# Kernel tuning notes

Hardware: AMD Instinct MI355X
Metric: run time of the kernel (lower is better)

The kernel has to match this reference:

```python
import jax, jax.numpy as jnp
import numpy as np

D_MODEL = 2048
N_HEADS = 16
N_KV_HEADS = 4
HEAD_DIM = D_MODEL // N_HEADS
KV_DIM = N_KV_HEADS * HEAD_DIM
EPS = 1e-6


def setup_inputs() -> dict:
    key = jax.random.key(0)
    ks = jax.random.split(key, 5)
    N, L = 4, 2048
    x = jax.random.normal(ks[0], (N, L, D_MODEL), dtype=jnp.float32)
    Wqkv = jax.random.normal(ks[1], (D_MODEL, D_MODEL + 2 * KV_DIM), dtype=jnp.float32) * (1.0 / np.sqrt(D_MODEL))
    bqkv = jnp.zeros((D_MODEL + 2 * KV_DIM,), dtype=jnp.float32)
    Wout = jax.random.normal(ks[2], (D_MODEL, D_MODEL), dtype=jnp.float32) * (1.0 / np.sqrt(D_MODEL))
    bout = jnp.zeros((D_MODEL,), dtype=jnp.float32)
    q_scale = jnp.ones((HEAD_DIM,), dtype=jnp.float32)
    k_scale = jnp.ones((HEAD_DIM,), dtype=jnp.float32)
    return {"x": x, "Wqkv": Wqkv, "bqkv": bqkv, "q_scale": q_scale, "k_scale": k_scale, "Wout": Wout, "bout": bout}


def _rmsnorm(x, scale):
    return x * (scale / jnp.sqrt(jnp.mean(jnp.square(x), axis=-1, keepdims=True) + EPS))


def reference(x, Wqkv, bqkv, q_scale, k_scale, Wout, bout):
    N, L, D = x.shape
    qkv = x @ Wqkv + bqkv  # [N, L, D + 2*kv_dim]
    q = qkv[..., :D].reshape(N, L, N_HEADS, HEAD_DIM).transpose(0, 2, 1, 3)          # [N,H,L,hd]
    k = qkv[..., D:D + KV_DIM].reshape(N, L, N_KV_HEADS, HEAD_DIM).transpose(0, 2, 1, 3)  # [N,Hkv,L,hd]
    v = qkv[..., D + KV_DIM:].reshape(N, L, N_KV_HEADS, HEAD_DIM).transpose(0, 2, 1, 3)
    q = _rmsnorm(q, q_scale)
    k = _rmsnorm(k, k_scale)
    # GQA expand (repeat_interleave over head dim)
    n_rep = N_HEADS // N_KV_HEADS
    k = jnp.repeat(k, n_rep, axis=1)
    v = jnp.repeat(v, n_rep, axis=1)
    scale = 1.0 / jnp.sqrt(jnp.float32(HEAD_DIM))
    scores = jnp.einsum("nhqd,nhkd->nhqk", q, k) * scale  # [N,H,L,L]
    causal = jnp.tril(jnp.ones((L, L), dtype=bool))
    scores = jnp.where(causal, scores, jnp.finfo(scores.dtype).min)
    attn = jax.nn.softmax(scores, axis=-1)
    y = jnp.einsum("nhqk,nhkd->nhqd", attn, v)  # [N,H,L,hd]
    y = y.transpose(0, 2, 1, 3).reshape(N, L, D)
    return y @ Wout + bout
```

## Files before the change

kernel.cpp:

```cpp
#include <hip/hip_runtime.h>

typedef unsigned int uint_t;
typedef unsigned short ushort_t;

using f32x4 = __attribute__((ext_vector_type(4))) float;
using bf16x8 = __attribute__((ext_vector_type(8))) short;

#define D_MODEL 2048
#define N_HEADS 16
#define N_KV    4
#define HD      128
#define KV_DIM  (N_KV * HD)
#define NQKV    (D_MODEL + 2*KV_DIM)
#define SEQ     2048
#define NB      4
#define MROWS   (NB * SEQ)
#define SM_SCALE 0.08838834764831845f

__device__ __forceinline__ ushort_t f2bf(float f) {
    uint_t u = __float_as_uint(f);
    u = (u + 0x7FFFu + ((u >> 16) & 1u)) >> 16;
    return (ushort_t)u;
}
__device__ __forceinline__ float bf2f(ushort_t h) {
    return __uint_as_float(((uint_t)h) << 16);
}

__device__ __forceinline__ void gload16(const ushort_t* g, ushort_t* l) {
    __builtin_amdgcn_global_load_lds(
        (const __attribute__((address_space(1))) unsigned int*)g,
        (__attribute__((address_space(3))) unsigned int*)l, 16, 0, 0);
}

__global__ __launch_bounds__(256) void conv_x_kernel(const float* __restrict__ in,
                                                     ushort_t* __restrict__ out, int n) {
    int i = (blockIdx.x * 256 + threadIdx.x) * 4;
    if (i >= n) return;
    float4 v = *(const float4*)&in[i];
    ushort_t o[4] = {f2bf(v.x), f2bf(v.y), f2bf(v.z), f2bf(v.w)};
    *(uint2*)&out[i] = *(uint2*)o;
}

__global__ __launch_bounds__(256) void conv_wt_kernel(const float* __restrict__ W,
                                                      ushort_t* __restrict__ WT,
                                                      int K, int Nout) {
    __shared__ float tile[32][33];
    int n0 = blockIdx.x * 32, k0 = blockIdx.y * 32;
    int tx = threadIdx.x, ty = threadIdx.y;
    for (int i = 0; i < 4; ++i)
        tile[ty + 8*i][tx] = W[(size_t)(k0 + ty + 8*i) * Nout + n0 + tx];
    __syncthreads();
    for (int i = 0; i < 4; ++i)
        WT[(size_t)(n0 + ty + 8*i) * K + k0 + tx] = f2bf(tile[tx][ty + 8*i]);
}

__global__ __launch_bounds__(256) void vt_kernel(const ushort_t* __restrict__ qkv,
                                                 ushort_t* __restrict__ Vt) {
    __shared__ ushort_t tile[64][72];
    int l0 = blockIdx.x * 64, d0 = blockIdx.y * 64;
    int nk = blockIdx.z;
    int n = nk >> 2, kvh = nk & 3;
    int t = threadIdx.x;
    const int coff = 2560 + kvh * 128 + d0;
    for (int i = 0; i < 2; ++i) {
        int idx = t + i * 256;
        int rr = idx >> 3, c = idx & 7;
        uint4 v = *(const uint4*)&qkv[(size_t)(n * SEQ + l0 + rr) * NQKV + coff + c * 8];
        *(uint4*)&tile[rr][c * 8] = v;
    }
    __syncthreads();
    for (int i = 0; i < 2; ++i) {
        int idx = t + i * 256;
        int dr = idx >> 3, c2 = idx & 7;
        ushort_t o[8];
        for (int j = 0; j < 8; ++j) o[j] = tile[c2 * 8 + j][dr];
        *(uint4*)&Vt[((size_t)nk * HD + d0 + dr) * SEQ + l0 + c2 * 8] = *(uint4*)o;
    }
}

template <bool OUT_BF16>
__global__ __launch_bounds__(256) void gemm_bt_kernel(const ushort_t* __restrict__ A,
                                                      const ushort_t* __restrict__ BT,
                                                      const float* __restrict__ bias,
                                                      void* __restrict__ C,
                                                      int M, int N, int K) {
    __shared__ ushort_t As[128][64];
    __shared__ ushort_t Bs[128][64];
    const int bm = blockIdx.x * 128, bn = blockIdx.y * 128;
    const int t = threadIdx.x;
    const int w = t >> 6, lane = t & 63, quad = lane >> 4, r = lane & 15;
    const int mb = (w >> 1) * 64, nb = (w & 1) * 64;

    f32x4 acc[4][4] = {};

    for (int k0 = 0; k0 < K; k0 += 64) {
        for (int i = 0; i < 4; ++i) {
            int ci = (w * 4 + i) * 64 + lane;
            int row = ci >> 3, c = ci & 7, cg = c ^ (row & 7);
            gload16(&A [(size_t)(bm + row) * K + k0 + cg * 8], &As[0][0] + (w * 4 + i) * 512);
            gload16(&BT[(size_t)(bn + row) * K + k0 + cg * 8], &Bs[0][0] + (w * 4 + i) * 512);
        }
        __syncthreads();
        for (int kk = 0; kk < 64; kk += 32) {
            bf16x8 af[4], bfr[4];
            int k4 = kk >> 3;
            for (int i = 0; i < 4; ++i)
                af[i]  = *(const bf16x8*)&As[mb + i * 16 + r][((k4 + quad) ^ (r & 7)) * 8];
            for (int j = 0; j < 4; ++j)
                bfr[j] = *(const bf16x8*)&Bs[nb + j * 16 + r][((k4 + quad) ^ (r & 7)) * 8];
            for (int i = 0; i < 4; ++i)
                for (int j = 0; j < 4; ++j)
                    acc[i][j] = __builtin_amdgcn_mfma_f32_16x16x32_bf16(af[i], bfr[j], acc[i][j], 0, 0, 0);
        }
        __syncthreads();
    }
    for (int i = 0; i < 4; ++i)
        for (int j = 0; j < 4; ++j)
            for (int reg = 0; reg < 4; ++reg) {
                int row = bm + mb + i * 16 + quad * 4 + reg;
                int col = bn + nb + j * 16 + r;
                float v = acc[i][j][reg] + bias[col];
                if (OUT_BF16) ((ushort_t*)C)[(size_t)row * N + col] = f2bf(v);
                else          ((float*)C)[(size_t)row * N + col] = v;
            }
}

__global__ __launch_bounds__(256) void rms_rearrange_kernel(const ushort_t* __restrict__ qkv,
                                                            const float* __restrict__ q_scale,
                                                            const float* __restrict__ k_scale,
                                                            ushort_t* __restrict__ Q,
                                                            ushort_t* __restrict__ Kb) {
    int rid = blockIdx.x;
    int n = rid >> 11, l = rid & 2047;
    int w = threadIdx.x >> 6, lane = threadIdx.x & 63;
    const ushort_t* rowp = qkv + (size_t)rid * NQKV;
    int d0 = lane * 2;
    for (int g = w; g < 20; g += 4) {
        uint_t pair = *(const uint_t*)&rowp[g * 128 + d0];
        float v0 = bf2f((ushort_t)(pair & 0xffff));
        float v1 = bf2f((ushort_t)(pair >> 16));
        float ss = v0 * v0 + v1 * v1;
        for (int m = 1; m < 64; m <<= 1) ss += __shfl_xor(ss, m);
        float inv = rsqrtf(ss * (1.0f / 128.0f) + 1e-6f);
        ushort_t* base;
        size_t dst;
        if (g < 16) {
            inv *= SM_SCALE;
            v0 *= inv * q_scale[d0];
            v1 *= inv * q_scale[d0 + 1];
            base = Q;  dst = (((size_t)(n * 16 + g) * SEQ + l) * HD + d0);
        } else {
            v0 *= inv * k_scale[d0];
            v1 *= inv * k_scale[d0 + 1];
            base = Kb; dst = (((size_t)(n * 4 + (g - 16)) * SEQ + l) * HD + d0);
        }
        uint_t op = (uint_t)f2bf(v0) | ((uint_t)f2bf(v1) << 16);
        *(uint_t*)&base[dst] = op;
    }
}

__global__ __launch_bounds__(256, 4) void attn_kernel(const ushort_t* __restrict__ Q,
                                                      const ushort_t* __restrict__ K,
                                                      const ushort_t* __restrict__ Vt,
                                                      ushort_t* __restrict__ Y) {
    const int pid = blockIdx.x, h = blockIdx.y, n = blockIdx.z;
    const int kvh = h >> 2;
    const ushort_t* Qp = Q  + (size_t)(n * N_HEADS + h) * SEQ * HD;
    const ushort_t* Kp = K  + (size_t)(n * N_KV + kvh) * SEQ * HD;
    const ushort_t* Vp = Vt + (size_t)(n * N_KV + kvh) * HD * SEQ;

    __shared__ ushort_t Ks[64][128];
    __shared__ ushort_t Vts[128][64];
    __shared__ ushort_t Ps[64][64];

    const int t = threadIdx.x, w = t >> 6, lane = t & 63, quad = lane >> 4, r = lane & 15;

    for (int rep = 0; rep < 2; ++rep) {
        const int qt = rep ? (31 - pid) : pid;
        __syncthreads();
        for (int i = 0; i < 4; ++i) {
            int ci = (w * 4 + i) * 64 + lane;
            int row = ci >> 4, c = ci & 15, cg = c ^ (row & 7);
            gload16(&Qp[(size_t)(qt * 64 + row) * HD + cg * 8], &Ks[0][0] + (w * 4 + i) * 512);
        }
        __syncthreads();
        bf16x8 aq[4];
        for (int kc = 0; kc < 4; ++kc)
            aq[kc] = *(const bf16x8*)&Ks[w * 16 + r][((kc * 4 + quad) ^ (r & 7)) * 8];

        f32x4 oacc[8] = {};
        float lsum[4] = {0.f, 0.f, 0.f, 0.f};

        for (int ct = 0; ct <= qt; ++ct) {
            __syncthreads();
            for (int i = 0; i < 4; ++i) {
                int ci = (w * 4 + i) * 64 + lane;
                {
                    int row = ci >> 4, c = ci & 15, cg = c ^ (row & 7);
                    gload16(&Kp[(size_t)(ct * 64 + row) * HD + cg * 8], &Ks[0][0] + (w * 4 + i) * 512);
                }
                {
                    int row = ci >> 3, c = ci & 7, cg = c ^ (row & 7);
                    gload16(&Vp[(size_t)row * SEQ + ct * 64 + cg * 8], &Vts[0][0] + (w * 4 + i) * 512);
                }
            }
            __syncthreads();

            f32x4 sacc[4] = {};
            for (int kc = 0; kc < 4; ++kc)
                for (int jt = 0; jt < 4; ++jt) {
                    bf16x8 bk = *(const bf16x8*)&Ks[jt * 16 + r][((kc * 4 + quad) ^ (r & 7)) * 8];
                    sacc[jt] = __builtin_amdgcn_mfma_f32_16x16x32_bf16(aq[kc], bk, sacc[jt], 0, 0, 0);
                }

            const bool diag = (ct == qt);
            for (int reg = 0; reg < 4; ++reg) {
                int prow = w * 16 + quad * 4 + reg;
                int qrow = prow;
                float rsum = 0.f;
                for (int jt = 0; jt < 4; ++jt) {
                    float s = sacc[jt][reg];
                    if (diag && (jt * 16 + r) > qrow) s = -1e30f;
                    float p = __expf(s);
                    ushort_t pb = f2bf(p);
                    rsum += bf2f(pb);
                    Ps[prow][(jt * 16 + r) ^ (quad << 4)] = pb;
                }
                lsum[reg] += rsum;
            }

            for (int kk = 0; kk < 64; kk += 32) {
                int prow = w * 16 + r;
                bf16x8 pa = *(const bf16x8*)&Ps[prow][(kk + quad * 8) ^ ((((r >> 2) & 3)) << 4)];
                for (int dt = 0; dt < 8; ++dt) {
                    bf16x8 bv = *(const bf16x8*)&Vts[dt * 16 + r][(((kk >> 3) + quad) ^ (r & 7)) * 8];
                    oacc[dt] = __builtin_amdgcn_mfma_f32_16x16x32_bf16(pa, bv, oacc[dt], 0, 0, 0);
                }
            }
        }

        for (int reg = 0; reg < 4; ++reg) {
            float s = lsum[reg];
            for (int m = 1; m < 16; m <<= 1) s += __shfl_xor(s, m);
            float invl = 1.0f / s;
            int lrow = qt * 64 + w * 16 + quad * 4 + reg;
            size_t base = ((size_t)(n * SEQ + lrow)) * D_MODEL + h * HD;
            for (int dt = 0; dt < 8; ++dt)
                Y[base + dt * 16 + r] = f2bf(oacc[dt][reg] * invl);
        }
    }
}

extern "C" void kernel_launch(void* const* d_in, const int* in_sizes, int n_in,
                              void* d_out, int out_size, void* d_ws, size_t ws_size,
                              hipStream_t stream) {
    const float* x       = (const float*)d_in[0];
    const float* Wqkv    = (const float*)d_in[1];
    const float* bqkv    = (const float*)d_in[2];
    const float* q_scale = (const float*)d_in[3];
    const float* k_scale = (const float*)d_in[4];
    const float* Wout    = (const float*)d_in[5];
    const float* bout    = (const float*)d_in[6];
    float* out = (float*)d_out;

    ushort_t* xb  = (ushort_t*)d_ws;
    ushort_t* WT  = xb  + (size_t)MROWS * D_MODEL;
    ushort_t* qkv = WT  + (size_t)NQKV * D_MODEL;
    ushort_t* Qb  = qkv + (size_t)MROWS * NQKV;
    ushort_t* Kb  = Qb  + (size_t)NB * N_HEADS * SEQ * HD;
    ushort_t* Vtb = Kb  + (size_t)NB * N_KV * SEQ * HD;

    conv_x_kernel<<<MROWS * D_MODEL / 1024, 256, 0, stream>>>(x, xb, MROWS * D_MODEL);
    conv_wt_kernel<<<dim3(NQKV / 32, D_MODEL / 32), dim3(32, 8), 0, stream>>>(Wqkv, WT, D_MODEL, NQKV);
    gemm_bt_kernel<true><<<dim3(MROWS / 128, NQKV / 128), 256, 0, stream>>>(xb, WT, bqkv, qkv, MROWS, NQKV, D_MODEL);
    rms_rearrange_kernel<<<MROWS, 256, 0, stream>>>(qkv, q_scale, k_scale, Qb, Kb);
    vt_kernel<<<dim3(SEQ / 64, HD / 64, NB * N_KV), 256, 0, stream>>>(qkv, Vtb);
    conv_wt_kernel<<<dim3(D_MODEL / 32, D_MODEL / 32), dim3(32, 8), 0, stream>>>(Wout, WT, D_MODEL, D_MODEL);
    attn_kernel<<<dim3(16, N_HEADS, NB), 256, 0, stream>>>(Qb, Kb, Vtb, xb);
    gemm_bt_kernel<false><<<dim3(MROWS / 128, D_MODEL / 128), 256, 0, stream>>>(xb, WT, bout, out, MROWS, D_MODEL, D_MODEL);
}
```

Measured before the change: 500.7 us.

## Fuse RMSNorm into QKV GEMM epilogue and widen attention Q tile to 128 rows

The QKV GEMM epilogue now adds the bias, computes per-head RMS norms across the two column-warps through shared memory, and writes Q, K and an untransposed V straight into head-major buffers. This removes the separate rms_rearrange pass and the round trip of the full bf16 qkv buffer. The attention kernel now handles 128 query rows per block, with each warp owning two 16-row slices, so every K/V tile loaded into LDS is reused twice. In exchange it uses more registers and lowers the occupancy hint to 2, and the row sum now uses the unrounded fp32 p values instead of the bf16-rounded ones.

Measured after the change: 474.9 us. 1.05x faster.

```diff
diff --git a/kernel.cpp b/kernel.cpp
--- a/kernel.cpp
+++ b/kernel.cpp
@@ -21,9 +21,6 @@
     uint_t u = __float_as_uint(f);
     u = (u + 0x7FFFu + ((u >> 16) & 1u)) >> 16;
     return (ushort_t)u;
-}
-__device__ __forceinline__ float bf2f(ushort_t h) {
-    return __uint_as_float(((uint_t)h) << 16);
 }
 
 __device__ __forceinline__ void gload16(const ushort_t* g, ushort_t* l) {
@@ -54,18 +51,16 @@
         WT[(size_t)(n0 + ty + 8*i) * K + k0 + tx] = f2bf(tile[tx][ty + 8*i]);
 }
 
-__global__ __launch_bounds__(256) void vt_kernel(const ushort_t* __restrict__ qkv,
+__global__ __launch_bounds__(256) void vt_kernel(const ushort_t* __restrict__ Vn,
                                                  ushort_t* __restrict__ Vt) {
     __shared__ ushort_t tile[64][72];
     int l0 = blockIdx.x * 64, d0 = blockIdx.y * 64;
     int nk = blockIdx.z;
-    int n = nk >> 2, kvh = nk & 3;
     int t = threadIdx.x;
-    const int coff = 2560 + kvh * 128 + d0;
     for (int i = 0; i < 2; ++i) {
         int idx = t + i * 256;
         int rr = idx >> 3, c = idx & 7;
-        uint4 v = *(const uint4*)&qkv[(size_t)(n * SEQ + l0 + rr) * NQKV + coff + c * 8];
+        uint4 v = *(const uint4*)&Vn[((size_t)nk * SEQ + l0 + rr) * HD + d0 + c * 8];
         *(uint4*)&tile[rr][c * 8] = v;
     }
     __syncthreads();
@@ -78,11 +73,33 @@
     }
 }
 
-template <bool OUT_BF16>
+#define GEMM_MAIN_LOOP(A, BT, K)                                                   \
+    for (int k0 = 0; k0 < K; k0 += 64) {                                           \
+        for (int i = 0; i < 4; ++i) {                                              \
+            int ci = (w * 4 + i) * 64 + lane;                                      \
+            int row = ci >> 3, c = ci & 7, cg = c ^ (row & 7);                     \
+            gload16(&A [(size_t)(bm + row) * K + k0 + cg * 8], &As[0][0] + (w * 4 + i) * 512); \
+            gload16(&BT[(size_t)(bn + row) * K + k0 + cg * 8], &Bs[0][0] + (w * 4 + i) * 512); \
+        }                                                                          \
+        __syncthreads();                                                           \
+        for (int kk = 0; kk < 64; kk += 32) {                                      \
+            bf16x8 af[4], bfr[4];                                                  \
+            int k4 = kk >> 3;                                                      \
+            for (int i = 0; i < 4; ++i)                                            \
+                af[i]  = *(const bf16x8*)&As[mb + i * 16 + r][((k4 + quad) ^ (r & 7)) * 8]; \
+            for (int j = 0; j < 4; ++j)                                            \
+                bfr[j] = *(const bf16x8*)&Bs[nb + j * 16 + r][((k4 + quad) ^ (r & 7)) * 8]; \
+            for (int i = 0; i < 4; ++i)                                            \
+                for (int j = 0; j < 4; ++j)                                        \
+                    acc[i][j] = __builtin_amdgcn_mfma_f32_16x16x32_bf16(af[i], bfr[j], acc[i][j], 0, 0, 0); \
+        }                                                                          \
+        __syncthreads();                                                           \
+    }
+
 __global__ __launch_bounds__(256) void gemm_bt_kernel(const ushort_t* __restrict__ A,
                                                       const ushort_t* __restrict__ BT,
                                                       const float* __restrict__ bias,
-                                                      void* __restrict__ C,
+                                                      float* __restrict__ C,
                                                       int M, int N, int K) {
     __shared__ ushort_t As[128][64];
     __shared__ ushort_t Bs[128][64];
@@ -90,76 +107,85 @@
     const int t = threadIdx.x;
     const int w = t >> 6, lane = t & 63, quad = lane >> 4, r = lane & 15;
     const int mb = (w >> 1) * 64, nb = (w & 1) * 64;
-
     f32x4 acc[4][4] = {};
-
-    for (int k0 = 0; k0 < K; k0 += 64) {
-        for (int i = 0; i < 4; ++i) {
-            int ci = (w * 4 + i) * 64 + lane;
-            int row = ci >> 3, c = ci & 7, cg = c ^ (row & 7);
-            gload16(&A [(size_t)(bm + row) * K + k0 + cg * 8], &As[0][0] + (w * 4 + i) * 512);
-            gload16(&BT[(size_t)(bn + row) * K + k0 + cg * 8], &Bs[0][0] + (w * 4 + i) * 512);
-        }
-        __syncthreads();
-        for (int kk = 0; kk < 64; kk += 32) {
-            bf16x8 af[4], bfr[4];
-            int k4 = kk >> 3;
-            for (int i = 0; i < 4; ++i)
-                af[i]  = *(const bf16x8*)&As[mb + i * 16 + r][((k4 + quad) ^ (r & 7)) * 8];
-            for (int j = 0; j < 4; ++j)
-                bfr[j] = *(const bf16x8*)&Bs[nb + j * 16 + r][((k4 + quad) ^ (r & 7)) * 8];
-            for (int i = 0; i < 4; ++i)
-                for (int j = 0; j < 4; ++j)
-                    acc[i][j] = __builtin_amdgcn_mfma_f32_16x16x32_bf16(af[i], bfr[j], acc[i][j], 0, 0, 0);
-        }
-        __syncthreads();
-    }
+    GEMM_MAIN_LOOP(A, BT, K)
     for (int i = 0; i < 4; ++i)
         for (int j = 0; j < 4; ++j)
             for (int reg = 0; reg < 4; ++reg) {
                 int row = bm + mb + i * 16 + quad * 4 + reg;
                 int col = bn + nb + j * 16 + r;
-                float v = acc[i][j][reg] + bias[col];
-                if (OUT_BF16) ((ushort_t*)C)[(size_t)row * N + col] = f2bf(v);
-                else          ((float*)C)[(size_t)row * N + col] = v;
-            }
-}
-
-__global__ __launch_bounds__(256) void rms_rearrange_kernel(const ushort_t* __restrict__ qkv,
-                                                            const float* __restrict__ q_scale,
-                                                            const float* __restrict__ k_scale,
-                                                            ushort_t* __restrict__ Q,
-                                                            ushort_t* __restrict__ Kb) {
-    int rid = blockIdx.x;
-    int n = rid >> 11, l = rid & 2047;
-    int w = threadIdx.x >> 6, lane = threadIdx.x & 63;
-    const ushort_t* rowp = qkv + (size_t)rid * NQKV;
-    int d0 = lane * 2;
-    for (int g = w; g < 20; g += 4) {
-        uint_t pair = *(const uint_t*)&rowp[g * 128 + d0];
-        float v0 = bf2f((ushort_t)(pair & 0xffff));
-        float v1 = bf2f((ushort_t)(pair >> 16));
-        float ss = v0 * v0 + v1 * v1;
-        for (int m = 1; m < 64; m <<= 1) ss += __shfl_xor(ss, m);
-        float inv = rsqrtf(ss * (1.0f / 128.0f) + 1e-6f);
-        ushort_t* base;
-        size_t dst;
-        if (g < 16) {
-            inv *= SM_SCALE;
-            v0 *= inv * q_scale[d0];
-            v1 *= inv * q_scale[d0 + 1];
-            base = Q;  dst = (((size_t)(n * 16 + g) * SEQ + l) * HD + d0);
-        } else {
-            v0 *= inv * k_scale[d0];
-            v1 *= inv * k_scale[d0 + 1];
-            base = Kb; dst = (((size_t)(n * 4 + (g - 16)) * SEQ + l) * HD + d0);
-        }
-        uint_t op = (uint_t)f2bf(v0) | ((uint_t)f2bf(v1) << 16);
-        *(uint_t*)&base[dst] = op;
-    }
-}
-
-__global__ __launch_bounds__(256, 4) void attn_kernel(const ushort_t* __restrict__ Q,
+                C[(size_t)row * N + col] = acc[i][j][reg] + bias[col];
+            }
+}
+
+__global__ __launch_bounds__(256) void gemm_qkv_kernel(const ushort_t* __restrict__ A,
+                                                       const ushort_t* __restrict__ BT,
+                                                       const float* __restrict__ bias,
+                                                       const float* __restrict__ q_scale,
+                                                       const float* __restrict__ k_scale,
+                                                       ushort_t* __restrict__ Q,
+                                                       ushort_t* __restrict__ Kb,
+                                                       ushort_t* __restrict__ Vn) {
+    __shared__ ushort_t As[128][64];
+    __shared__ ushort_t Bs[128][64];
+    __shared__ float ssum[2][128];
+    const int K = D_MODEL;
+    const int bm = blockIdx.x * 128, bn = blockIdx.y * 128;
+    const int t = threadIdx.x;
+    const int w = t >> 6, lane = t & 63, quad = lane >> 4, r = lane & 15;
+    const int mb = (w >> 1) * 64, nb = (w & 1) * 64;
+    f32x4 acc[4][4] = {};
+    GEMM_MAIN_LOOP(A, BT, K)
+
+    const int g = blockIdx.y;
+    float bj[4];
+    for (int j = 0; j < 4; ++j) bj[j] = bias[bn + nb + j * 16 + r];
+    for (int i = 0; i < 4; ++i)
+        for (int j = 0; j < 4; ++j)
+            for (int reg = 0; reg < 4; ++reg) acc[i][j][reg] += bj[j];
+
+    const int n = bm >> 11, lb = bm & 2047;
+    if (g < 20) {
+        for (int i = 0; i < 4; ++i)
+            for (int reg = 0; reg < 4; ++reg) {
+                float p = 0.f;
+                for (int j = 0; j < 4; ++j) p += acc[i][j][reg] * acc[i][j][reg];
+                p += __shfl_xor(p, 1); p += __shfl_xor(p, 2);
+                p += __shfl_xor(p, 4); p += __shfl_xor(p, 8);
+                if (r == 0) ssum[w & 1][mb + i * 16 + quad * 4 + reg] = p;
+            }
+        __syncthreads();
+        const float* scp = (g < 16) ? q_scale : k_scale;
+        const float smul = (g < 16) ? SM_SCALE : 1.0f;
+        float scj[4];
+        for (int j = 0; j < 4; ++j) scj[j] = scp[nb + j * 16 + r];
+        ushort_t* dst = (g < 16) ? (Q  + (size_t)(n * 16 + g) * SEQ * HD)
+                                 : (Kb + (size_t)(n * 4 + g - 16) * SEQ * HD);
+        for (int i = 0; i < 4; ++i)
+            for (int reg = 0; reg < 4; ++reg) {
+                int rl = mb + i * 16 + quad * 4 + reg;
+                float ss = ssum[0][rl] + ssum[1][rl];
+                float iv = rsqrtf(ss * (1.0f / 128.0f) + 1e-6f) * smul;
+                size_t lrow = lb + rl;
+                for (int j = 0; j < 4; ++j) {
+                    int d = nb + j * 16 + r;
+                    dst[lrow * HD + d] = f2bf(acc[i][j][reg] * iv * scj[j]);
+                }
+            }
+    } else {
+        ushort_t* dst = Vn + (size_t)(n * 4 + g - 20) * SEQ * HD;
+        for (int i = 0; i < 4; ++i)
+            for (int reg = 0; reg < 4; ++reg) {
+                size_t lrow = lb + mb + i * 16 + quad * 4 + reg;
+                for (int j = 0; j < 4; ++j) {
+                    int d = nb + j * 16 + r;
+                    dst[lrow * HD + d] = f2bf(acc[i][j][reg]);
+                }
+            }
+    }
+}
+
+__global__ __launch_bounds__(256, 2) void attn_kernel(const ushort_t* __restrict__ Q,
                                                       const ushort_t* __restrict__ K,
                                                       const ushort_t* __restrict__ Vt,
                                                       ushort_t* __restrict__ Y) {
@@ -171,27 +197,24 @@
 
     __shared__ ushort_t Ks[64][128];
     __shared__ ushort_t Vts[128][64];
-    __shared__ ushort_t Ps[64][64];
+    __shared__ ushort_t Ps[128][64];
 
     const int t = threadIdx.x, w = t >> 6, lane = t & 63, quad = lane >> 4, r = lane & 15;
 
     for (int rep = 0; rep < 2; ++rep) {
-        const int qt = rep ? (31 - pid) : pid;
-        __syncthreads();
-        for (int i = 0; i < 4; ++i) {
-            int ci = (w * 4 + i) * 64 + lane;
-            int row = ci >> 4, c = ci & 15, cg = c ^ (row & 7);
-            gload16(&Qp[(size_t)(qt * 64 + row) * HD + cg * 8], &Ks[0][0] + (w * 4 + i) * 512);
-        }
-        __syncthreads();
-        bf16x8 aq[4];
-        for (int kc = 0; kc < 4; ++kc)
-            aq[kc] = *(const bf16x8*)&Ks[w * 16 + r][((kc * 4 + quad) ^ (r & 7)) * 8];
-
-        f32x4 oacc[8] = {};
-        float lsum[4] = {0.f, 0.f, 0.f, 0.f};
-
-        for (int ct = 0; ct <= qt; ++ct) {
+        const int qt = rep ? (15 - pid) : pid;
+        const int q0 = qt * 128;
+
+        bf16x8 aq[2][4];
+        for (int s = 0; s < 2; ++s)
+            for (int kc = 0; kc < 4; ++kc)
+                aq[s][kc] = *(const bf16x8*)&Qp[(size_t)(q0 + w * 32 + s * 16 + r) * HD + kc * 32 + quad * 8];
+
+        f32x4 oacc[2][8] = {};
+        float lsum[2][4] = {};
+        const int nct = 2 * qt + 2;
+
+        for (int ct = 0; ct < nct; ++ct) {
             __syncthreads();
             for (int i = 0; i < 4; ++i) {
                 int ci = (w * 4 + i) * 64 + lane;
@@ -206,48 +229,52 @@
             }
             __syncthreads();
 
-            f32x4 sacc[4] = {};
+            f32x4 sacc[2][4] = {};
             for (int kc = 0; kc < 4; ++kc)
                 for (int jt = 0; jt < 4; ++jt) {
                     bf16x8 bk = *(const bf16x8*)&Ks[jt * 16 + r][((kc * 4 + quad) ^ (r & 7)) * 8];
-                    sacc[jt] = __builtin_amdgcn_mfma_f32_16x16x32_bf16(aq[kc], bk, sacc[jt], 0, 0, 0);
-                }
-
-            const bool diag = (ct == qt);
-            for (int reg = 0; reg < 4; ++reg) {
-                int prow = w * 16 + quad * 4 + reg;
-                int qrow = prow;
-                float rsum = 0.f;
-                for (int jt = 0; jt < 4; ++jt) {
-                    float s = sacc[jt][reg];
-                    if (diag && (jt * 16 + r) > qrow) s = -1e30f;
-                    float p = __expf(s);
-                    ushort_t pb = f2bf(p);
-                    rsum += bf2f(pb);
-                    Ps[prow][(jt * 16 + r) ^ (quad << 4)] = pb;
-                }
-                lsum[reg] += rsum;
-            }
+                    sacc[0][jt] = __builtin_amdgcn_mfma_f32_16x16x32_bf16(aq[0][kc], bk, sacc[0][jt], 0, 0, 0);
+                    sacc[1][jt] = __builtin_amdgcn_mfma_f32_16x16x32_bf16(aq[1][kc], bk, sacc[1][jt], 0, 0, 0);
+                }
+
+            const bool diag = (ct >= 2 * qt);
+            for (int s = 0; s < 2; ++s)
+                for (int reg = 0; reg < 4; ++reg) {
+                    int prow = w * 32 + s * 16 + quad * 4 + reg;
+                    int qg = q0 + prow;
+                    float rs = 0.f;
+                    for (int jt = 0; jt < 4; ++jt) {
+                        float sv = sacc[s][jt][reg];
+                        if (diag && (ct * 64 + jt * 16 + r) > qg) sv = -1e30f;
+                        float p = __expf(sv);
+                        rs += p;
+                        Ps[prow][(jt * 16 + r) ^ (quad << 4)] = (ushort_t)(__float_as_uint(p) >> 16);
+                    }
+                    lsum[s][reg] += rs;
+                }
 
             for (int kk = 0; kk < 64; kk += 32) {
-                int prow = w * 16 + r;
-                bf16x8 pa = *(const bf16x8*)&Ps[prow][(kk + quad * 8) ^ ((((r >> 2) & 3)) << 4)];
+                bf16x8 pa[2];
+                for (int s = 0; s < 2; ++s)
+                    pa[s] = *(const bf16x8*)&Ps[w * 32 + s * 16 + r][(kk + quad * 8) ^ (((r >> 2) & 3) << 4)];
                 for (int dt = 0; dt < 8; ++dt) {
                     bf16x8 bv = *(const bf16x8*)&Vts[dt * 16 + r][(((kk >> 3) + quad) ^ (r & 7)) * 8];
-                    oacc[dt] = __builtin_amdgcn_mfma_f32_16x16x32_bf16(pa, bv, oacc[dt], 0, 0, 0);
+                    oacc[0][dt] = __builtin_amdgcn_mfma_f32_16x16x32_bf16(pa[0], bv, oacc[0][dt], 0, 0, 0);
+                    oacc[1][dt] = __builtin_amdgcn_mfma_f32_16x16x32_bf16(pa[1], bv, oacc[1][dt], 0, 0, 0);
                 }
             }
         }
 
-        for (int reg = 0; reg < 4; ++reg) {
-            float s = lsum[reg];
-            for (int m = 1; m < 16; m <<= 1) s += __shfl_xor(s, m);
-            float invl = 1.0f / s;
-            int lrow = qt * 64 + w * 16 + quad * 4 + reg;
-            size_t base = ((size_t)(n * SEQ + lrow)) * D_MODEL + h * HD;
-            for (int dt = 0; dt < 8; ++dt)
-                Y[base + dt * 16 + r] = f2bf(oacc[dt][reg] * invl);
-        }
+        for (int s = 0; s < 2; ++s)
+            for (int reg = 0; reg < 4; ++reg) {
+                float sv = lsum[s][reg];
+                for (int m = 1; m < 16; m <<= 1) sv += __shfl_xor(sv, m);
+                float invl = 1.0f / sv;
+                int lrow = q0 + w * 32 + s * 16 + quad * 4 + reg;
+                size_t base = ((size_t)(n * SEQ + lrow)) * D_MODEL + h * HD;
+                for (int dt = 0; dt < 8; ++dt)
+                    Y[base + dt * 16 + r] = f2bf(oacc[s][dt][reg] * invl);
+            }
     }
 }
 
@@ -265,17 +292,16 @@
 
     ushort_t* xb  = (ushort_t*)d_ws;
     ushort_t* WT  = xb  + (size_t)MROWS * D_MODEL;
-    ushort_t* qkv = WT  + (size_t)NQKV * D_MODEL;
-    ushort_t* Qb  = qkv + (size_t)MROWS * NQKV;
+    ushort_t* Qb  = WT  + (size_t)NQKV * D_MODEL;
     ushort_t* Kb  = Qb  + (size_t)NB * N_HEADS * SEQ * HD;
-    ushort_t* Vtb = Kb  + (size_t)NB * N_KV * SEQ * HD;
+    ushort_t* Vnb = Kb  + (size_t)NB * N_KV * SEQ * HD;
+    ushort_t* Vtb = Vnb + (size_t)NB * N_KV * SEQ * HD;
 
     conv_x_kernel<<<MROWS * D_MODEL / 1024, 256, 0, stream>>>(x, xb, MROWS * D_MODEL);
     conv_wt_kernel<<<dim3(NQKV / 32, D_MODEL / 32), dim3(32, 8), 0, stream>>>(Wqkv, WT, D_MODEL, NQKV);
-    gemm_bt_kernel<true><<<dim3(MROWS / 128, NQKV / 128), 256, 0, stream>>>(xb, WT, bqkv, qkv, MROWS, NQKV, D_MODEL);
-    rms_rearrange_kernel<<<MROWS, 256, 0, stream>>>(qkv, q_scale, k_scale, Qb, Kb);
-    vt_kernel<<<dim3(SEQ / 64, HD / 64, NB * N_KV), 256, 0, stream>>>(qkv, Vtb);
+    gemm_qkv_kernel<<<dim3(MROWS / 128, NQKV / 128), 256, 0, stream>>>(xb, WT, bqkv, q_scale, k_scale, Qb, Kb, Vnb);
+    vt_kernel<<<dim3(SEQ / 64, HD / 64, NB * N_KV), 256, 0, stream>>>(Vnb, Vtb);
     conv_wt_kernel<<<dim3(D_MODEL / 32, D_MODEL / 32), dim3(32, 8), 0, stream>>>(Wout, WT, D_MODEL, D_MODEL);
-    attn_kernel<<<dim3(16, N_HEADS, NB), 256, 0, stream>>>(Qb, Kb, Vtb, xb);
-    gemm_bt_kernel<false><<<dim3(MROWS / 128, D_MODEL / 128), 256, 0, stream>>>(xb, WT, bout, out, MROWS, D_MODEL, D_MODEL);
-}
+    attn_kernel<<<dim3(8, N_HEADS, NB), 256, 0, stream>>>(Qb, Kb, Vtb, xb);
+    gemm_bt_kernel<<<dim3(MROWS / 128, D_MODEL / 128), 256, 0, stream>>>(xb, WT, bout, out, MROWS, D_MODEL, D_MODEL);
+}
```
